# Kernel optimization log

Hardware: AMD Instinct MI355X
Metric: run time of the kernel (lower is better)

## Reference

```python
import jax, jax.numpy as jnp
from jax import lax
import numpy as np

K = 3       # kernel_size
STRIDE = 1
PAD = 1
DIL = 1


def setup_inputs() -> dict:
    key = jax.random.key(0)
    k1, k2, k3, k4 = jax.random.split(key, 4)
    B, C, H, W, Co = 8, 128, 64, 64, 128
    x = jax.random.normal(k1, (B, C, H, W), jnp.float32)
    # offset conv: deformable_groups * 2 * K * K = 18 output channels
    w_off = jax.random.normal(k2, (2 * K * K, C, K, K), jnp.float32) * 0.01
    b_off = jax.random.normal(k3, (2 * K * K,), jnp.float32) * 0.01
    w_dcn = jax.random.normal(k4, (Co, C, K, K), jnp.float32) * (1.0 / np.sqrt(C * K * K))
    return {"x": x, "w_off": w_off, "b_off": b_off, "w_dcn": w_dcn}


def _deform_conv(x, w_off, b_off, w_dcn):
    B, C, H, W = x.shape
    Ho = (H + 2 * PAD - DIL * (K - 1) - 1) // STRIDE + 1
    Wo = (W + 2 * PAD - DIL * (K - 1) - 1) // STRIDE + 1
    KK = K * K

    # --- offset branch: standard conv2d ---
    offset = lax.conv_general_dilated(
        x, w_off, window_strides=(STRIDE, STRIDE),
        padding=[(PAD, PAD), (PAD, PAD)], rhs_dilation=(DIL, DIL),
        dimension_numbers=("NCHW", "OIHW", "NCHW"))
    offset = offset + b_off[None, :, None, None]          # [B, 2*KK, Ho, Wo]
    off = offset.reshape(B, KK, 2, Ho, Wo)
    dy, dx = off[:, :, 0], off[:, :, 1]                   # [B, KK, Ho, Wo]

    # --- sampling coordinates: p0 + p_k + offset ---
    ky, kx = jnp.meshgrid(jnp.arange(K), jnp.arange(K), indexing="ij")
    ky = (ky.reshape(-1) * DIL).astype(x.dtype)           # [KK]
    kx = (kx.reshape(-1) * DIL).astype(x.dtype)
    base_y = (jnp.arange(Ho) * STRIDE - PAD).astype(x.dtype)[None, :, None] + ky[:, None, None]
    base_x = (jnp.arange(Wo) * STRIDE - PAD).astype(x.dtype)[None, None, :] + kx[:, None, None]
    y = base_y[None] + dy                                 # [B, KK, Ho, Wo]
    xc = base_x[None] + dx

    y0 = jnp.floor(y)
    x0 = jnp.floor(xc)
    wy = y - y0                                           # bilinear weights
    wx = xc - x0
    y0i = y0.astype(jnp.int32)
    x0i = x0.astype(jnp.int32)

    def sample_one(xb, y0i, x0i, wy, wx):
        # xb: [C, H, W]; index tensors: [KK, Ho, Wo]
        xf = xb.reshape(C, H * W)

        def corner(iy, ix):
            valid = (iy >= 0) & (iy < H) & (ix >= 0) & (ix < W)   # zero padding
            idx = jnp.clip(iy, 0, H - 1) * W + jnp.clip(ix, 0, W - 1)
            v = jnp.take(xf, idx.reshape(-1), axis=1).reshape(C, KK, Ho, Wo)
            return v * valid[None].astype(xb.dtype)

        v00 = corner(y0i, x0i)
        v01 = corner(y0i, x0i + 1)
        v10 = corner(y0i + 1, x0i)
        v11 = corner(y0i + 1, x0i + 1)
        return (v00 * (1 - wy) * (1 - wx) + v01 * (1 - wy) * wx
                + v10 * wy * (1 - wx) + v11 * wy * wx)      # [C, KK, Ho, Wo]

    sampled = jax.vmap(sample_one)(x, y0i, x0i, wy, wx)      # [B, C, KK, Ho, Wo]

    # --- deformable conv accumulation (groups=1, no bias) ---
    w = w_dcn.reshape(w_dcn.shape[0], C, KK)
    return jnp.einsum("bckhw,ock->bohw", sampled, w)


def reference(x, w_off, b_off, w_dcn):
    return _deform_conv(x, w_off, b_off, w_dcn)
```

## Files before the change

kernel.cpp:

```cpp
#include <hip/hip_runtime.h>

typedef float f32x2 __attribute__((ext_vector_type(2)));
typedef float f32x4 __attribute__((ext_vector_type(4)));
typedef int   i32x4 __attribute__((ext_vector_type(4)));
typedef unsigned u32x4 __attribute__((ext_vector_type(4)));
typedef short b16x8 __attribute__((ext_vector_type(8)));

#define BAR_LGKM() asm volatile("s_waitcnt lgkmcnt(0)\n\ts_barrier" ::: "memory")

__device__ __forceinline__ short f2b(float v) {
  union { float f; unsigned u; } x; x.f = v;
  unsigned r = x.u + 0x7FFFu + ((x.u >> 16) & 1u);
  return (short)(r >> 16);
}
__device__ __forceinline__ float b2f(short s) {
  union { unsigned u; float f; } x; x.u = ((unsigned)(unsigned short)s) << 16;
  return x.f;
}
__device__ __forceinline__ f32x2 up2(int d) {
  union { unsigned u; float f; } a, b;
  a.u = (unsigned)d << 16;
  b.u = (unsigned)d & 0xffff0000u;
  f32x2 r; r[0] = a.f; r[1] = b.f; return r;
}

#define WT_ELEMS   (9 * 128 * 128)
#define WOFF_ELEMS (9 * 32 * 128)
#define XT_BYTES   (8u * 4096u * 128u * 2u)

#define WIN_OFF   0
#define SS0_OFF   23040
#define SS1_OFF   27136
#define COFS_OFF  31232
#define WTA_OFF   35840
#define ARENA_SZ  40448

__global__ __launch_bounds__(256) void prep_all(
    const float* __restrict__ xg, const float* __restrict__ w_off,
    const float* __restrict__ w_dcn,
    short* __restrict__ xt, short* __restrict__ wT, short* __restrict__ wOffT)
{
  __shared__ float tile[32][65];
  const int bid = blockIdx.x;
  const int t   = threadIdx.x;

  if (bid < 512) {
    const int b = bid >> 6, y = bid & 63;
    const float* src = xg + ((size_t)b << 19) + y * 64;
    short*       dst = xt + ((size_t)b << 19) + (size_t)y * 8192;

    for (int ct = 0; ct < 4; ++ct) {
      __syncthreads();
      int c_l = t >> 3, w0 = (t & 7) * 8;
      const float* p = src + (size_t)(ct * 32 + c_l) * 4096 + w0;
      f32x4 a0 = *(const f32x4*)p;
      f32x4 a1 = *(const f32x4*)(p + 4);
      #pragma unroll
      for (int i = 0; i < 4; ++i) { tile[c_l][w0 + i] = a0[i]; tile[c_l][w0 + 4 + i] = a1[i]; }
      __syncthreads();
      int w = t >> 2, j0 = (t & 3) * 8;
      b16x8 pk;
      #pragma unroll
      for (int j = 0; j < 8; ++j) pk[j] = f2b(tile[j0 + j][w]);
      *(b16x8*)(dst + w * 128 + ct * 32 + j0) = pk;
    }
  } else {
    int tt = (bid - 512) * 256 + t;
    int stride = 64 * 256;
    for (int i = tt; i < WT_ELEMS; i += stride) {
      int j    = i & 7;
      int lane = (i >> 3) & 63;
      int kk   = (i >> 9) & 3;
      int og   = (i >> 11) & 7;
      int k    = i >> 14;
      int o = og * 16 + (lane & 15);
      int c = kk * 32 + (lane >> 4) * 8 + j;
      wT[i] = f2b(w_dcn[o * 1152 + c * 9 + k]);
    }
    for (int i = tt; i < WOFF_ELEMS; i += stride) {
      int j    = i & 7;
      int lane = (i >> 3) & 63;
      int kk   = (i >> 9) & 3;
      int fo   = (i >> 11) & 1;
      int k    = i >> 12;
      int o = fo * 16 + (lane & 15);
      int c = kk * 32 + (lane >> 4) * 8 + j;
      wOffT[i] = (o < 18) ? f2b(w_off[o * 1152 + c * 9 + k]) : (short)0;
    }
  }
}

__device__ __forceinline__ void lerp_half(char* sbuf, const char* win, const short* xb,
                                          int h, const unsigned* cofsT, const f32x4* wtA,
                                          int k, int px_s, int cg) {
  u32x4 co = *(const u32x4*)&cofsT[(k * 32 + px_s) * 4];
  f32x4 wv = wtA[k * 32 + px_s];
  i32x4 g[4];
  #pragma unroll
  for (int c = 0; c < 4; ++c) {
    unsigned ofs = co[c];
    if (ofs & 0x80000000u) {
      const short* gp = xb + (size_t)(ofs & 0x7fffffffu) * 128 + h * 64 + cg * 8;
      g[c] = *(const i32x4*)gp;
    } else {
      unsigned key = ((ofs >> 7) & 7) << 4;
      g[c] = *(const i32x4*)(win + ofs + ((cg * 16) ^ key));
    }
  }
  f32x2 w0p; w0p[0] = wv[0]; w0p[1] = wv[0];
  f32x2 w1p; w1p[0] = wv[1]; w1p[1] = wv[1];
  f32x2 w2p; w2p[0] = wv[2]; w2p[1] = wv[2];
  f32x2 w3p; w3p[0] = wv[3]; w3p[1] = wv[3];
  i32x4 pk;
  #pragma unroll
  for (int d = 0; d < 4; ++d) {
    f32x2 acc = up2(g[0][d]) * w0p;
    acc += up2(g[1][d]) * w1p;
    acc += up2(g[2][d]) * w2p;
    acc += up2(g[3][d]) * w3p;
    int r;
    asm("v_cvt_pk_bf16_f32 %0, %1, %2" : "=v"(r) : "v"(acc[0]), "v"(acc[1]));
    pk[d] = r;
  }
  *(i32x4*)(sbuf + px_s * 128 + ((cg * 16) ^ ((px_s & 7) << 4))) = pk;
}

__device__ __forceinline__ void load_wfrag_half(b16x8 (&w)[4], const short* wT,
                                                int k, int h, int wv_, int lane) {
  const int og0 = wv_ * 2;
  #pragma unroll
  for (int kkl = 0; kkl < 2; ++kkl) {
    w[kkl]     = *(const b16x8*)(wT + ((((k * 8 + og0)     * 4) + 2 * h + kkl) << 9) + lane * 8);
    w[2 + kkl] = *(const b16x8*)(wT + ((((k * 8 + og0 + 1) * 4) + 2 * h + kkl) << 9) + lane * 8);
  }
}

__device__ __forceinline__ void mfma_half(const char* sbuf, const b16x8 (&w)[4],
                                          int l15, int l4,
                                          f32x4& a00, f32x4& a01, f32x4& a10, f32x4& a11) {
  #pragma unroll
  for (int kkl = 0; kkl < 2; ++kkl) {
    int cl2 = kkl * 64 + l4 * 16;
    b16x8 b0 = *(const b16x8*)(sbuf + l15 * 128        + (cl2 ^ ((l15 & 7) << 4)));
    b16x8 b1 = *(const b16x8*)(sbuf + (16 + l15) * 128 + (cl2 ^ ((l15 & 7) << 4)));
    a00 = __builtin_amdgcn_mfma_f32_16x16x32_bf16(w[kkl],     b0, a00, 0, 0, 0);
    a01 = __builtin_amdgcn_mfma_f32_16x16x32_bf16(w[kkl],     b1, a01, 0, 0, 0);
    a10 = __builtin_amdgcn_mfma_f32_16x16x32_bf16(w[2 + kkl], b0, a10, 0, 0, 0);
    a11 = __builtin_amdgcn_mfma_f32_16x16x32_bf16(w[2 + kkl], b1, a11, 0, 0, 0);
  }
}

__global__ __launch_bounds__(256, 4) void dcn_mfma(
    const short* __restrict__ xt, const float* __restrict__ b_off,
    const short* __restrict__ wT, const short* __restrict__ wOffT,
    float* __restrict__ out)
{
  __shared__ __align__(16) char arena[ARENA_SZ];

  char*     sW    = arena + WIN_OFF;
  char*     win   = arena + WIN_OFF;
  char*     sS0   = arena + SS0_OFF;
  char*     sS1   = arena + SS1_OFF;
  float*    offT  = (float*)(arena + SS0_OFF);
  unsigned* cofsT = (unsigned*)(arena + COFS_OFF);
  f32x4*    wtA   = (f32x4*)(arena + WTA_OFF);

  const int tid  = threadIdx.x;
  const int lane = tid & 63;
  const int wv_  = tid >> 6;
  const int bid  = blockIdx.x;
  const int swz  = (bid & 7) * 128 + (bid >> 3);
  const int b    = swz >> 7;
  const int ho   = (swz >> 1) & 63;
  const int wo0  = (swz & 1) * 32;

  const int px_s = tid >> 3;
  const int cg   = tid & 7;
  const int l15  = lane & 15;
  const int l4   = lane >> 4;

  const short* xb = xt + ((size_t)b << 19);

  #pragma unroll 1
  for (int i = 0; i < 7; ++i) {
    int s = tid + i * 256;
    if (s < 1632) {
      int p = s >> 4, cc = s & 15;
      int py = p / 34, pxw = p - py * 34;
      int y = ho - 1 + py, xw = wo0 + pxw - 1;
      bool v = ((unsigned)y < 64u) && ((unsigned)xw < 64u);
      b16x8 q = {0,0,0,0,0,0,0,0};
      if (v) q = *(const b16x8*)(xb + ((size_t)(y * 64 + xw) << 7) + cc * 8);
      *(b16x8*)(sW + p * 256 + ((cc * 16) ^ ((p & 7) << 4))) = q;
    }
  }
  __syncthreads();

  f32x4 accP = {0.f, 0.f, 0.f, 0.f};
  const int fo = wv_ >> 1, fp = wv_ & 1;
  {
    const int bpx = fp * 16 + l15;
    #pragma unroll 1
    for (int k = 0; k < 9; ++k) {
      int ky = k / 3, kx = k - ky * 3;
      int p  = ky * 34 + bpx + kx;
      const short* wkf = wOffT + (((k * 2 + fo) * 4) << 9);
      #pragma unroll
      for (int kk = 0; kk < 4; ++kk) {
        int cf = kk * 32 + l4 * 8;
        b16x8 a  = *(const b16x8*)(wkf + (kk << 9) + lane * 8);
        b16x8 bb = *(const b16x8*)(sW + p * 256 + ((cf * 2) ^ ((p & 7) << 4)));
        accP = __builtin_amdgcn_mfma_f32_16x16x32_bf16(a, bb, accP, 0, 0, 0);
      }
    }
  }
  __syncthreads();
  {
    int px = fp * 16 + l15;
    int ob = fo * 16 + l4 * 4;
    #pragma unroll
    for (int r = 0; r < 4; ++r)
      offT[(ob + r) * 32 + px] = accP[r];
  }
  __syncthreads();

  #pragma unroll 1
  for (int i = 0; i < 2; ++i) {
    int item = tid + i * 256;
    if (item < 288) {
      int k = item >> 5, px = item & 31;
      int ky = k / 3, kx = k - ky * 3;
      float dy = offT[(2 * k) * 32 + px]     + b_off[2 * k];
      float dx = offT[(2 * k + 1) * 32 + px] + b_off[2 * k + 1];
      float yy = (float)(ho - 1 + ky) + dy;
      float xx = (float)(wo0 + px - 1 + kx) + dx;
      float y0f = floorf(yy), x0f = floorf(xx);
      float wy = yy - y0f, wx = xx - x0f;
      int y0 = (int)y0f, x0 = (int)x0f;
      int y1 = y0 + 1, x1 = x0 + 1;
      int cy0 = min(max(y0, 0), 63), cx0 = min(max(x0, 0), 63);
      int cy1 = min(max(y1, 0), 63), cx1 = min(max(x1, 0), 63);
      float vy0 = ((unsigned)y0 < 64u) ? 1.f : 0.f;
      float vy1 = ((unsigned)y1 < 64u) ? 1.f : 0.f;
      float vx0 = ((unsigned)x0 < 64u) ? 1.f : 0.f;
      float vx1 = ((unsigned)x1 < 64u) ? 1.f : 0.f;
      f32x4 wvv;
      wvv[0] = (1.f - wy) * (1.f - wx) * vy0 * vx0;
      wvv[1] = (1.f - wy) * wx         * vy0 * vx1;
      wvv[2] = wy         * (1.f - wx) * vy1 * vx0;
      wvv[3] = wy         * wx         * vy1 * vx1;
      int cys[4] = {cy0, cy0, cy1, cy1};
      int cxs[4] = {cx0, cx1, cx0, cx1};
      u32x4 enc;
      #pragma unroll
      for (int c = 0; c < 4; ++c) {
        int wr = cys[c] - (ho - 2);
        int wc = cxs[c] - (wo0 - 2);
        bool inw = ((unsigned)wr < 5u) && ((unsigned)wc < 36u);
        enc[c] = inw ? (unsigned)((wr * 36 + wc) * 128)
                     : (0x80000000u | (unsigned)(cys[c] * 64 + cxs[c]));
      }
      *(u32x4*)&cofsT[item * 4] = enc;
      wtA[item] = wvv;
    }
  }
  __syncthreads();

  f32x4 acc00 = {0,0,0,0}, acc01 = {0,0,0,0}, acc10 = {0,0,0,0}, acc11 = {0,0,0,0};
  b16x8 wreg[4], wnext[4];
  load_wfrag_half(wreg, wT, 0, 0, wv_, lane);

  #pragma unroll 1
  for (int h = 0; h < 2; ++h) {
    #pragma unroll 1
    for (int i = 0; i < 6; ++i) {
      int s = tid + i * 256;
      if (s < 1440) {
        int seg = s & 7, pos = s >> 3;
        int r = pos / 36, cc = pos - r * 36;
        int y = ho - 2 + r, x = wo0 - 2 + cc;
        bool v = ((unsigned)y < 64u) && ((unsigned)x < 64u);
        b16x8 q = {0,0,0,0,0,0,0,0};
        if (v) q = *(const b16x8*)(xb + ((size_t)(y * 64 + x) << 7) + h * 64 + seg * 8);
        *(b16x8*)(win + pos * 128 + ((seg * 16) ^ ((pos & 7) << 4))) = q;
      }
    }
    BAR_LGKM();

    #pragma unroll 1
    for (int k = 0; k < 9; ++k) {
      char* sb = ((h * 9 + k) & 1) ? sS1 : sS0;
      lerp_half(sb, win, xb, h, cofsT, wtA, k, px_s, cg);
      if (k < 8)            load_wfrag_half(wnext, wT, k + 1, h, wv_, lane);
      else if (h == 0)      load_wfrag_half(wnext, wT, 0, 1, wv_, lane);
      BAR_LGKM();
      mfma_half(sb, wreg, l15, l4, acc00, acc01, acc10, acc11);
      #pragma unroll
      for (int i = 0; i < 4; ++i) wreg[i] = wnext[i];
    }
  }

  {
    size_t base = ((size_t)b * 128) * 4096 + (size_t)ho * 64 + wo0;
    int o0 = wv_ * 32 + l4 * 4;
    #pragma unroll
    for (int r = 0; r < 4; ++r) {
      out[base + (size_t)(o0 + r) * 4096 + l15]           = acc00[r];
      out[base + (size_t)(o0 + r) * 4096 + 16 + l15]      = acc01[r];
      out[base + (size_t)(o0 + 16 + r) * 4096 + l15]      = acc10[r];
      out[base + (size_t)(o0 + 16 + r) * 4096 + 16 + l15] = acc11[r];
    }
  }
}

extern "C" void kernel_launch(void* const* d_in, const int* in_sizes, int n_in,
                              void* d_out, int out_size, void* d_ws, size_t ws_size,
                              hipStream_t stream) {
  const float* x     = (const float*)d_in[0];
  const float* w_off = (const float*)d_in[1];
  const float* b_off = (const float*)d_in[2];
  const float* w_dcn = (const float*)d_in[3];
  float* out = (float*)d_out;

  short* xt    = (short*)d_ws;
  short* wT    = (short*)((char*)d_ws + XT_BYTES);
  short* wOffT = (short*)((char*)d_ws + XT_BYTES + WT_ELEMS * 2);

  hipLaunchKernelGGL(prep_all, dim3(576),  dim3(256), 0, stream,
                     x, w_off, w_dcn, xt, wT, wOffT);
  hipLaunchKernelGGL(dcn_mfma, dim3(1024), dim3(256), 0, stream, xt, b_off, wT, wOffT, out);
}
```

Before: 45.63 us.

## Shrink DCN tile to 16 output pixels with 128-thread blocks

Each block now covers 16 output pixels with 2 waves instead of 32 pixels with 4 waves, which doubles the grid to 2048 blocks. Every wave computes 64 output channels by 16 pixels, using 8 weight fragments and 4 accumulators. The LDS arena shrinks to about 22KB so more blocks can be resident per CU, and the offset tile gets its own region. The cost is more halo overhead per pixel: window loads go from 36 to 20 columns for 16 pixels, and the offset conv is recomputed over larger relative halos. Register pressure also rises from the doubled weight fragments.

```diff
diff --git a/kernel.cpp b/kernel.cpp
--- a/kernel.cpp
+++ b/kernel.cpp
@@ -29,11 +29,12 @@
 #define XT_BYTES   (8u * 4096u * 128u * 2u)
 
 #define WIN_OFF   0
-#define SS0_OFF   23040
-#define SS1_OFF   27136
-#define COFS_OFF  31232
-#define WTA_OFF   35840
-#define ARENA_SZ  40448
+#define SS0_OFF   12800
+#define SS1_OFF   14848
+#define COFS_OFF  16896
+#define WTA_OFF   19200
+#define OFFT_OFF  21504
+#define ARENA_SZ  22656
 
 __global__ __launch_bounds__(256) void prep_all(
     const float* __restrict__ xg, const float* __restrict__ w_off,
@@ -93,8 +94,8 @@
 __device__ __forceinline__ void lerp_half(char* sbuf, const char* win, const short* xb,
                                           int h, const unsigned* cofsT, const f32x4* wtA,
                                           int k, int px_s, int cg) {
-  u32x4 co = *(const u32x4*)&cofsT[(k * 32 + px_s) * 4];
-  f32x4 wv = wtA[k * 32 + px_s];
+  u32x4 co = *(const u32x4*)&cofsT[(k * 16 + px_s) * 4];
+  f32x4 wv = wtA[k * 16 + px_s];
   i32x4 g[4];
   #pragma unroll
   for (int c = 0; c < 4; ++c) {
@@ -125,32 +126,30 @@
   *(i32x4*)(sbuf + px_s * 128 + ((cg * 16) ^ ((px_s & 7) << 4))) = pk;
 }
 
-__device__ __forceinline__ void load_wfrag_half(b16x8 (&w)[4], const short* wT,
+__device__ __forceinline__ void load_wfrag_half(b16x8 (&w)[8], const short* wT,
                                                 int k, int h, int wv_, int lane) {
-  const int og0 = wv_ * 2;
+  const int og0 = wv_ * 4;
   #pragma unroll
-  for (int kkl = 0; kkl < 2; ++kkl) {
-    w[kkl]     = *(const b16x8*)(wT + ((((k * 8 + og0)     * 4) + 2 * h + kkl) << 9) + lane * 8);
-    w[2 + kkl] = *(const b16x8*)(wT + ((((k * 8 + og0 + 1) * 4) + 2 * h + kkl) << 9) + lane * 8);
-  }
-}
-
-__device__ __forceinline__ void mfma_half(const char* sbuf, const b16x8 (&w)[4],
-                                          int l15, int l4,
-                                          f32x4& a00, f32x4& a01, f32x4& a10, f32x4& a11) {
+  for (int og = 0; og < 4; ++og)
+    #pragma unroll
+    for (int kkl = 0; kkl < 2; ++kkl)
+      w[og * 2 + kkl] =
+        *(const b16x8*)(wT + ((((k * 8 + og0 + og) * 4) + 2 * h + kkl) << 9) + lane * 8);
+}
+
+__device__ __forceinline__ void mfma_half(const char* sbuf, const b16x8 (&w)[8],
+                                          int l15, int l4, f32x4 (&acc)[4]) {
   #pragma unroll
   for (int kkl = 0; kkl < 2; ++kkl) {
     int cl2 = kkl * 64 + l4 * 16;
-    b16x8 b0 = *(const b16x8*)(sbuf + l15 * 128        + (cl2 ^ ((l15 & 7) << 4)));
-    b16x8 b1 = *(const b16x8*)(sbuf + (16 + l15) * 128 + (cl2 ^ ((l15 & 7) << 4)));
-    a00 = __builtin_amdgcn_mfma_f32_16x16x32_bf16(w[kkl],     b0, a00, 0, 0, 0);
-    a01 = __builtin_amdgcn_mfma_f32_16x16x32_bf16(w[kkl],     b1, a01, 0, 0, 0);
-    a10 = __builtin_amdgcn_mfma_f32_16x16x32_bf16(w[2 + kkl], b0, a10, 0, 0, 0);
-    a11 = __builtin_amdgcn_mfma_f32_16x16x32_bf16(w[2 + kkl], b1, a11, 0, 0, 0);
-  }
-}
-
-__global__ __launch_bounds__(256, 4) void dcn_mfma(
+    b16x8 b0 = *(const b16x8*)(sbuf + l15 * 128 + (cl2 ^ ((l15 & 7) << 4)));
+    #pragma unroll
+    for (int og = 0; og < 4; ++og)
+      acc[og] = __builtin_amdgcn_mfma_f32_16x16x32_bf16(w[og * 2 + kkl], b0, acc[og], 0, 0, 0);
+  }
+}
+
+__global__ __launch_bounds__(128, 4) void dcn_mfma(
     const short* __restrict__ xt, const float* __restrict__ b_off,
     const short* __restrict__ wT, const short* __restrict__ wOffT,
     float* __restrict__ out)
@@ -161,18 +160,18 @@
   char*     win   = arena + WIN_OFF;
   char*     sS0   = arena + SS0_OFF;
   char*     sS1   = arena + SS1_OFF;
-  float*    offT  = (float*)(arena + SS0_OFF);
   unsigned* cofsT = (unsigned*)(arena + COFS_OFF);
   f32x4*    wtA   = (f32x4*)(arena + WTA_OFF);
+  float*    offT  = (float*)(arena + OFFT_OFF);
 
   const int tid  = threadIdx.x;
   const int lane = tid & 63;
   const int wv_  = tid >> 6;
   const int bid  = blockIdx.x;
-  const int swz  = (bid & 7) * 128 + (bid >> 3);
-  const int b    = swz >> 7;
-  const int ho   = (swz >> 1) & 63;
-  const int wo0  = (swz & 1) * 32;
+  const int swz  = (bid & 7) * 256 + (bid >> 3);
+  const int b    = swz >> 8;
+  const int ho   = (swz >> 2) & 63;
+  const int wo0  = (swz & 3) * 16;
 
   const int px_s = tid >> 3;
   const int cg   = tid & 7;
@@ -183,10 +182,10 @@
 
   #pragma unroll 1
   for (int i = 0; i < 7; ++i) {
-    int s = tid + i * 256;
-    if (s < 1632) {
+    int s = tid + i * 128;
+    if (s < 864) {
       int p = s >> 4, cc = s & 15;
-      int py = p / 34, pxw = p - py * 34;
+      int py = p / 18, pxw = p - py * 18;
       int y = ho - 1 + py, xw = wo0 + pxw - 1;
       bool v = ((unsigned)y < 64u) && ((unsigned)xw < 64u);
       b16x8 q = {0,0,0,0,0,0,0,0};
@@ -197,13 +196,12 @@
   __syncthreads();
 
   f32x4 accP = {0.f, 0.f, 0.f, 0.f};
-  const int fo = wv_ >> 1, fp = wv_ & 1;
   {
-    const int bpx = fp * 16 + l15;
+    const int fo = wv_;
     #pragma unroll 1
     for (int k = 0; k < 9; ++k) {
       int ky = k / 3, kx = k - ky * 3;
-      int p  = ky * 34 + bpx + kx;
+      int p  = ky * 18 + l15 + kx;
       const short* wkf = wOffT + (((k * 2 + fo) * 4) << 9);
       #pragma unroll
       for (int kk = 0; kk < 4; ++kk) {
@@ -216,22 +214,23 @@
   }
   __syncthreads();
   {
-    int px = fp * 16 + l15;
-    int ob = fo * 16 + l4 * 4;
+    int o0 = wv_ * 16 + l4 * 4;
     #pragma unroll
-    for (int r = 0; r < 4; ++r)
-      offT[(ob + r) * 32 + px] = accP[r];
+    for (int r = 0; r < 4; ++r) {
+      int o = o0 + r;
+      if (o < 18) offT[o * 16 + l15] = accP[r];
+    }
   }
   __syncthreads();
 
   #pragma unroll 1
   for (int i = 0; i < 2; ++i) {
-    int item = tid + i * 256;
-    if (item < 288) {
-      int k = item >> 5, px = item & 31;
+    int item = tid + i * 128;
+    if (item < 144) {
+      int k = item >> 4, px = item & 15;
       int ky = k / 3, kx = k - ky * 3;
-      float dy = offT[(2 * k) * 32 + px]     + b_off[2 * k];
-      float dx = offT[(2 * k + 1) * 32 + px] + b_off[2 * k + 1];
+      float dy = offT[(2 * k) * 16 + px]     + b_off[2 * k];
+      float dx = offT[(2 * k + 1) * 16 + px] + b_off[2 * k + 1];
       float yy = (float)(ho - 1 + ky) + dy;
       float xx = (float)(wo0 + px - 1 + kx) + dx;
       float y0f = floorf(yy), x0f = floorf(xx);
@@ -256,8 +255,8 @@
       for (int c = 0; c < 4; ++c) {
         int wr = cys[c] - (ho - 2);
         int wc = cxs[c] - (wo0 - 2);
-        bool inw = ((unsigned)wr < 5u) && ((unsigned)wc < 36u);
-        enc[c] = inw ? (unsigned)((wr * 36 + wc) * 128)
+        bool inw = ((unsigned)wr < 5u) && ((unsigned)wc < 20u);
+        enc[c] = inw ? (unsigned)((wr * 20 + wc) * 128)
                      : (0x80000000u | (unsigned)(cys[c] * 64 + cxs[c]));
       }
       *(u32x4*)&cofsT[item * 4] = enc;
@@ -266,18 +265,18 @@
   }
   __syncthreads();
 
-  f32x4 acc00 = {0,0,0,0}, acc01 = {0,0,0,0}, acc10 = {0,0,0,0}, acc11 = {0,0,0,0};
-  b16x8 wreg[4], wnext[4];
+  f32x4 acc[4] = {{0,0,0,0}, {0,0,0,0}, {0,0,0,0}, {0,0,0,0}};
+  b16x8 wreg[8], wnext[8];
   load_wfrag_half(wreg, wT, 0, 0, wv_, lane);
 
   #pragma unroll 1
   for (int h = 0; h < 2; ++h) {
     #pragma unroll 1
-    for (int i = 0; i < 6; ++i) {
-      int s = tid + i * 256;
-      if (s < 1440) {
+    for (int i = 0; i < 7; ++i) {
+      int s = tid + i * 128;
+      if (s < 800) {
         int seg = s & 7, pos = s >> 3;
-        int r = pos / 36, cc = pos - r * 36;
+        int r = pos / 20, cc = pos - r * 20;
         int y = ho - 2 + r, x = wo0 - 2 + cc;
         bool v = ((unsigned)y < 64u) && ((unsigned)x < 64u);
         b16x8 q = {0,0,0,0,0,0,0,0};
@@ -294,21 +293,20 @@
       if (k < 8)            load_wfrag_half(wnext, wT, k + 1, h, wv_, lane);
       else if (h == 0)      load_wfrag_half(wnext, wT, 0, 1, wv_, lane);
       BAR_LGKM();
-      mfma_half(sb, wreg, l15, l4, acc00, acc01, acc10, acc11);
-      #pragma unroll
-      for (int i = 0; i < 4; ++i) wreg[i] = wnext[i];
+      mfma_half(sb, wreg, l15, l4, acc);
+      #pragma unroll
+      for (int i = 0; i < 8; ++i) wreg[i] = wnext[i];
     }
   }
 
   {
     size_t base = ((size_t)b * 128) * 4096 + (size_t)ho * 64 + wo0;
-    int o0 = wv_ * 32 + l4 * 4;
     #pragma unroll
-    for (int r = 0; r < 4; ++r) {
-      out[base + (size_t)(o0 + r) * 4096 + l15]           = acc00[r];
-      out[base + (size_t)(o0 + r) * 4096 + 16 + l15]      = acc01[r];
-      out[base + (size_t)(o0 + 16 + r) * 4096 + l15]      = acc10[r];
-      out[base + (size_t)(o0 + 16 + r) * 4096 + 16 + l15] = acc11[r];
+    for (int og = 0; og < 4; ++og) {
+      int o0 = wv_ * 64 + og * 16 + l4 * 4;
+      #pragma unroll
+      for (int r = 0; r < 4; ++r)
+        out[base + (size_t)(o0 + r) * 4096 + l15] = acc[og][r];
     }
   }
 }
@@ -328,5 +326,5 @@
 
   hipLaunchKernelGGL(prep_all, dim3(576),  dim3(256), 0, stream,
                      x, w_off, w_dcn, xt, wT, wOffT);
-  hipLaunchKernelGGL(dcn_mfma, dim3(1024), dim3(256), 0, stream, xt, b_off, wT, wOffT, out);
-}
+  hipLaunchKernelGGL(dcn_mfma, dim3(2048), dim3(128), 0, stream, xt, b_off, wT, wOffT, out);
+}
```

Measured after the change: 70.42 us. 54.3% more time.
